# Optimization experiments

Hardware: AMD Instinct MI355X
Metric: run time of the kernel (lower is better)

The kernel has to match this reference:

```python
import jax, jax.numpy as jnp
import numpy as np

B, CIN, H, W = 16, 128, 56, 56
COUT, KH, KW = 256, 3, 3
STRIDE = (1, 1)
PAD = ((1, 1), (1, 1))


def setup_inputs() -> dict:
    key = jax.random.key(0)
    k1, k2, k3 = jax.random.split(key, 3)
    x = jax.random.normal(k1, (B, CIN, H, W), dtype=jnp.float32)
    weight = jax.random.normal(k2, (COUT, CIN, KH, KW), dtype=jnp.float32) * 0.05
    bias = jax.random.normal(k3, (COUT,), dtype=jnp.float32)
    return {"x": x, "weight": weight, "bias": bias}


def reference(x, weight, bias):
    # Conv2d with zero padding, stride 1 -- identical math to the torch
    # unfold+expand+multiply+triple-sum path.
    dn = jax.lax.conv_dimension_numbers(x.shape, weight.shape, ("NCHW", "OIHW", "NCHW"))
    out = jax.lax.conv_general_dilated(x, weight, STRIDE, PAD, dimension_numbers=dn)
    out = out + bias[None, :, None, None]

    # Sparsity of the elementwise product patches * weight.
    # count_nonzero(x_patch * w) over all (b,hw,ww,co,ci,kh,kw) factorizes as
    # sum over windows of conv(1[x!=0], 1[w!=0]) -- same count without
    # materializing the [B,Hw,Ww,Co,Ci,kh,kw] tensor the torch code builds.
    co, ci, kh, kw = weight.shape
    hw, ww = out.shape[2], out.shape[3]
    num_elements = x.shape[0] * hw * ww * co * ci * kh * kw
    nz_map = jax.lax.conv_general_dilated(
        (x != 0).astype(jnp.float32),
        (weight != 0).astype(jnp.float32),
        STRIDE, PAD, dimension_numbers=dn)
    num_nonzero = jnp.sum(nz_map)
    layer_sparsity = (jnp.float32(num_elements) - num_nonzero) / jnp.float32(num_elements)
    return out, layer_sparsity
```

## Files before the change

### kernel.cpp

```cpp
#include <hip/hip_runtime.h>
#include <hip/hip_bf16.h>

typedef __attribute__((ext_vector_type(8))) short bf16x8;
typedef __attribute__((ext_vector_type(8))) unsigned short ushort8;
typedef __attribute__((ext_vector_type(4))) unsigned short ushort4v;
typedef __attribute__((ext_vector_type(4))) float f32x4;
typedef __attribute__((ext_vector_type(4))) unsigned int uint4v;

#define CIN_  128
#define BATCH 16
#define SP_   3136
#define CO_   256
#define NTOT  50176

#define XP_BYTES   13778944
#define WT_BYTES   589824
#define WS_NEEDED  14447104

__device__ __forceinline__ unsigned short f2bf(float f) {
    unsigned int u = __float_as_uint(f);
    u = (u + 0x7fffu + ((u >> 16) & 1u)) >> 16;
    return (unsigned short)u;
}

__device__ __forceinline__ void gl_lds16(const unsigned short* g, unsigned short* l) {
    __builtin_amdgcn_global_load_lds(
        (const __attribute__((address_space(1))) unsigned int*)g,
        (__attribute__((address_space(3))) unsigned int*)l, 16, 0, 0);
}

__global__ __launch_bounds__(256) void k_aux(
    const float* __restrict__ x, const float* __restrict__ w,
    unsigned short* __restrict__ Wt, unsigned short* __restrict__ xp,
    float* __restrict__ Wcnt, float* __restrict__ part)
{
    __shared__ float T[64][65];
    __shared__ float red9[4][9];
    const int blk = blockIdx.x;
    const int tid = threadIdx.x;

    if (blk < 288) {
        int base = (blk * 256 + tid) * 4;
        float4 v = *(const float4*)(w + base);
        #pragma unroll
        for (int j = 0; j < 4; ++j) {
            int e = base + j;
            int co = e / 1152;
            int r  = e - co * 1152;
            int ci = r / 9;
            int koff = r - ci * 9;
            Wt[(koff * 256 + co) * 128 + ci] = f2bf(((const float*)&v)[j]);
        }
    } else if (blk < 576) {
        int lane = tid & 63;
        int j = (blk - 288) * 4 + (tid >> 6);
        float c = 0.f;
        for (int co = lane; co < 256; co += 64)
            c += (w[(size_t)co * 1152 + j] != 0.0f) ? 1.f : 0.f;
        #pragma unroll
        for (int s = 32; s > 0; s >>= 1) c += __shfl_down(c, s, 64);
        if (lane == 0) Wcnt[j] = c;
    } else if (blk < 2624) {
        int bc = blk - 576;
        int ci = bc & 127;
        int b  = bc >> 7;
        const float* xpk = x + (size_t)bc * SP_;
        float cnt[9];
        #pragma unroll
        for (int k = 0; k < 9; ++k) cnt[k] = 0.f;
        for (int e = tid; e < SP_; e += 256) {
            float v = xpk[e];
            if (v != 0.f) {
                int h = e / 56, w_ = e - h * 56;
                float r0 = (h <= 54) ? 1.f : 0.f;
                float r2 = (h >= 1) ? 1.f : 0.f;
                float c0 = (w_ <= 54) ? 1.f : 0.f;
                float c2 = (w_ >= 1) ? 1.f : 0.f;
                cnt[0] += r0 * c0; cnt[1] += r0; cnt[2] += r0 * c2;
                cnt[3] += c0;      cnt[4] += 1.f; cnt[5] += c2;
                cnt[6] += r2 * c0; cnt[7] += r2; cnt[8] += r2 * c2;
            }
        }
        #pragma unroll
        for (int k = 0; k < 9; ++k) {
            #pragma unroll
            for (int s = 32; s > 0; s >>= 1) cnt[k] += __shfl_down(cnt[k], s, 64);
        }
        if ((tid & 63) == 0) {
            #pragma unroll
            for (int k = 0; k < 9; ++k) red9[tid >> 6][k] = cnt[k];
        }
        __syncthreads();
        if (tid < 9) {
            float s = red9[0][tid] + red9[1][tid] + red9[2][tid] + red9[3][tid];
            part[(ci * 9 + tid) * 16 + b] = s;
        }
    } else if (blk < 4192) {
        int i = blk - 2624;
        int sp0 = (i % 49) * 64;
        int rest = i / 49;
        int ci0 = (rest & 1) * 64;
        int b = rest >> 1;
        const float* xb = x + ((size_t)(b * 128 + ci0)) * SP_ + sp0;
        #pragma unroll
        for (int r = 0; r < 16; ++r) {
            const int ci_l = (tid >> 6) * 16 + r;
            const int sp_l = tid & 63;
            T[sp_l][ci_l] = xb[(size_t)ci_l * SP_ + sp_l];
        }
        __syncthreads();
        #pragma unroll
        for (int r = 0; r < 4; ++r) {
            const int sp_l = (tid >> 4) * 4 + r;
            const int cc   = (tid & 15) * 4;
            const int sp = sp0 + sp_l;
            const int oh = sp / 56, ow = sp - oh * 56;
            ushort4v v;
            #pragma unroll
            for (int j = 0; j < 4; ++j) v[j] = f2bf(T[sp_l][cc + j]);
            *(ushort4v*)&xp[(((size_t)b * 58 + oh + 1) * 58 + (ow + 1)) * 128 + ci0 + cc] = v;
        }
    } else {
        int b = blk - 4192;
        if (tid < 228) {
            int oh, ow;
            if (tid < 58)       { oh = 0;            ow = tid; }
            else if (tid < 116) { oh = 57;           ow = tid - 58; }
            else if (tid < 172) { oh = tid - 116 + 1; ow = 0; }
            else                { oh = tid - 172 + 1; ow = 57; }
            unsigned short* p = xp + (((size_t)b * 58 + oh) * 58 + ow) * 128;
            ushort8 z = {};
            #pragma unroll
            for (int j = 0; j < 16; ++j) *(ushort8*)(p + j * 8) = z;
        }
    }
}

__global__ void k_spars(const float* __restrict__ Wcnt, const float* __restrict__ part,
                        float* __restrict__ out_scalar) {
    __shared__ double red[256];
    int t = threadIdx.x;
    double s = 0.0;
    for (int j = t; j < 1152; j += 256) {
        const float4* p4 = (const float4*)(part + (size_t)j * 16);
        float4 a = p4[0], b = p4[1], c = p4[2], d = p4[3];
        float xs = (a.x + a.y + a.z + a.w) + (b.x + b.y + b.z + b.w)
                 + (c.x + c.y + c.z + c.w) + (d.x + d.y + d.z + d.w);
        s += (double)Wcnt[j] * (double)xs;
    }
    red[t] = s; __syncthreads();
    for (int k = 128; k > 0; k >>= 1) {
        if (t < k) red[t] += red[t + k];
        __syncthreads();
    }
    if (t == 0) {
        const double ne = 14797504512.0;
        out_scalar[0] = (float)((ne - red[0]) / ne);
    }
}

__global__ __launch_bounds__(512, 2) void k_conv8(
    const unsigned short* __restrict__ xp, const unsigned short* __restrict__ Wt,
    const float* __restrict__ bias, float* __restrict__ out)
{
    __shared__ __attribute__((aligned(16))) unsigned short Albs[2 * 16384];
    __shared__ __attribute__((aligned(16))) unsigned short Blbs[2 * 16384];

    const int tid  = threadIdx.x;
    const int lane = tid & 63;
    const int l15  = lane & 15;
    const int w    = tid >> 6;
    const int wm   = w >> 2;
    const int wn   = w & 3;
    const int n0   = blockIdx.x * 256;

    int xoffA[2], woffB[2];
    #pragma unroll
    for (int j = 0; j < 2; ++j) {
        int g   = j * 512 + tid;
        int row = g >> 2;
        int c   = (g & 3) ^ ((row >> 1) & 3);
        int n   = n0 + row;
        int b   = n / SP_;
        int sp  = n - b * SP_;
        int oh  = sp / 56, ow = sp - oh * 56;
        xoffA[j] = ((b * 58 + oh + 1) * 58 + (ow + 1)) * 128 + c * 8;
        woffB[j] = row * 128 + c * 8;
    }

    auto stageA = [&](int nb, int xsh, int s) {
        #pragma unroll
        for (int j = 0; j < 2; ++j)
            gl_lds16(xp + xsh + s * 32 + xoffA[j],
                     &Albs[nb + s * 8192 + (j * 512 + tid) * 8]);
    };
    auto stageB = [&](int nb, int wsh, int s) {
        #pragma unroll
        for (int j = 0; j < 2; ++j)
            gl_lds16(Wt + wsh + s * 32 + woffB[j],
                     &Blbs[nb + s * 8192 + (j * 512 + tid) * 8]);
    };

    f32x4 acc[8][4] = {};
    const int cl = lane >> 4;

#define LDA_(bo, S, R) \
    (*(const bf16x8*)&Albs[(bo) + (S) * 8192 + ((R) + l15) * 32 + \
        ((cl ^ ((((R) + l15) >> 1) & 3)) * 8)])
#define LDB_(bo, S, R) \
    (*(const bf16x8*)&Blbs[(bo) + (S) * 8192 + ((R) + l15) * 32 + \
        ((cl ^ ((((R) + l15) >> 1) & 3)) * 8)])

#define SUBPH(BO, S)                                                       \
    {                                                                      \
        bf16x8 b_[4], a_[8];                                               \
        _Pragma("unroll")                                                  \
        for (int nn = 0; nn < 4; ++nn) b_[nn] = LDB_(BO, S, wn * 64 + nn * 16);\
        _Pragma("unroll")                                                  \
        for (int m = 0; m < 8; ++m) a_[m] = LDA_(BO, S, wm * 128 + m * 16);\
        __builtin_amdgcn_s_setprio(1);                                     \
        _Pragma("unroll")                                                  \
        for (int m = 0; m < 8; ++m)                                        \
            _Pragma("unroll")                                              \
            for (int nn = 0; nn < 4; ++nn)                                 \
                acc[m][nn] = __builtin_amdgcn_mfma_f32_16x16x32_bf16(      \
                    a_[m], b_[nn], acc[m][nn], 0, 0, 0);                   \
        __builtin_amdgcn_s_setprio(0);                                     \
    }

    {
        const int xsh0 = (-59) * 128;
        stageA(0, xsh0, 0); stageB(0, 0, 0);
        stageA(0, xsh0, 1); stageB(0, 0, 1);
    }

    #pragma unroll 1
    for (int kt = 0; kt < 18; ++kt) {
        const int bo = (kt & 1) << 14;
        const int nb = 16384 - bo;

        asm volatile("s_waitcnt vmcnt(0)" ::: "memory");
        __builtin_amdgcn_s_barrier();

        if (kt < 17) {
            const int kn = kt + 1;
            const int koffn = kn >> 1;
            const int kdn = koffn / 3;
            const int xshn = ((kdn - 1) * 58 + (koffn - kdn * 3 - 1)) * 128 + (kn & 1) * 64;
            const int wshn = koffn * 32768 + (kn & 1) * 64;
            stageA(nb, xshn, 0); stageB(nb, wshn, 0);
            stageA(nb, xshn, 1); stageB(nb, wshn, 1);
        }

        SUBPH(bo, 0);
        SUBPH(bo, 1);
    }

#undef SUBPH
#undef LDA_
#undef LDB_

    #pragma unroll
    for (int m = 0; m < 8; ++m) {
        int n  = n0 + wm * 128 + m * 16 + (lane >> 4) * 4;
        int b  = n / SP_;
        int sp = n - b * SP_;
        #pragma unroll
        for (int nn = 0; nn < 4; ++nn) {
            int co = wn * 64 + nn * 16 + l15;
            f32x4 v = acc[m][nn] + bias[co];
            *(f32x4*)&out[((size_t)(b * CO_ + co)) * SP_ + sp] = v;
        }
    }
}

__global__ void k_wt(const float* __restrict__ w, unsigned short* __restrict__ Wt) {
    int e = blockIdx.x * 256 + threadIdx.x;
    float v = w[e];
    int co = e / 1152;
    int r  = e - co * 1152;
    int ci = r / 9;
    int koff = r - ci * 9;
    Wt[(koff * 256 + co) * 128 + ci] = f2bf(v);
}

__global__ void k_wcnt(const float* __restrict__ w, float* __restrict__ Wcnt) {
    int j = blockIdx.x;
    int lane = threadIdx.x;
    float c = 0.f;
    for (int co = lane; co < 256; co += 64)
        c += (w[(size_t)co * 1152 + j] != 0.0f) ? 1.f : 0.f;
    #pragma unroll
    for (int s = 32; s > 0; s >>= 1) c += __shfl_down(c, s, 64);
    if (lane == 0) Wcnt[j] = c;
}

__global__ void k_xcnt(const float* __restrict__ x, float* __restrict__ Xcnt) {
    int blk = blockIdx.x;
    int ci = blk & 127;
    const float* xpk = x + (size_t)blk * SP_;
    int tid = threadIdx.x;
    float cnt[9];
    #pragma unroll
    for (int k = 0; k < 9; ++k) cnt[k] = 0.f;
    for (int e = tid; e < SP_; e += 256) {
        float v = xpk[e];
        if (v != 0.f) {
            int h = e / 56, w_ = e - h * 56;
            float r0 = (h <= 54) ? 1.f : 0.f;
            float r2 = (h >= 1) ? 1.f : 0.f;
            float c0 = (w_ <= 54) ? 1.f : 0.f;
            float c2 = (w_ >= 1) ? 1.f : 0.f;
            cnt[0] += r0 * c0; cnt[1] += r0; cnt[2] += r0 * c2;
            cnt[3] += c0;      cnt[4] += 1.f; cnt[5] += c2;
            cnt[6] += r2 * c0; cnt[7] += r2; cnt[8] += r2 * c2;
        }
    }
    #pragma unroll
    for (int k = 0; k < 9; ++k) {
        #pragma unroll
        for (int s = 32; s > 0; s >>= 1) cnt[k] += __shfl_down(cnt[k], s, 64);
    }
    if ((tid & 63) == 0) {
        #pragma unroll
        for (int k = 0; k < 9; ++k)
            atomicAdd(&Xcnt[ci * 9 + k], cnt[k]);
    }
}

__global__ void k_spars_f(const float* __restrict__ Wcnt, const float* __restrict__ Xcnt,
                          float* __restrict__ out_scalar) {
    __shared__ double red[256];
    int t = threadIdx.x;
    double s = 0.0;
    for (int j = t; j < 1152; j += 256)
        s += (double)Wcnt[j] * (double)Xcnt[j];
    red[t] = s; __syncthreads();
    for (int k = 128; k > 0; k >>= 1) {
        if (t < k) red[t] += red[t + k];
        __syncthreads();
    }
    if (t == 0) {
        const double ne = 14797504512.0;
        out_scalar[0] = (float)((ne - red[0]) / ne);
    }
}

__global__ __launch_bounds__(256) void k_conv(
    const float* __restrict__ x, const unsigned short* __restrict__ Wt,
    const float* __restrict__ bias, float* __restrict__ out)
{
    __shared__ __attribute__((aligned(16))) unsigned short AldsF[64][40];
    __shared__ __attribute__((aligned(16))) unsigned short BldsF[64][40];

    const int tid  = threadIdx.x;
    const int lane = tid & 63;
    const int wid  = tid >> 6;
    const int wm   = wid >> 1, wn = wid & 1;

    const int n0  = blockIdx.x * 64;
    const int b   = blockIdx.x / 49;
    const int sp0 = n0 - b * SP_;
    const int co0 = blockIdx.y * 64;

    const int a_co = tid >> 2;
    const int a_ci = (tid & 3) * 8;
    const int b_n  = tid & 63;
    const int b_k0 = (tid >> 6) * 8;

    const int sp = sp0 + b_n;
    const int oh = sp / 56, ow = sp - oh * 56;

    f32x4 acc[2][2] = {};
    const float* xb_base = x + (size_t)b * CIN_ * SP_;

    for (int koff = 0; koff < 9; ++koff) {
        const int dh = koff / 3 - 1, dw = koff - (koff / 3) * 3 - 1;
        const int ih = oh + dh, iw = ow + dw;
        const bool valid = ((unsigned)ih < 56u) && ((unsigned)iw < 56u);
        const float* xb = xb_base + sp + dh * 56 + dw;
        const unsigned short* wp = Wt + ((size_t)(koff * 256 + co0 + a_co)) * 128 + a_ci;

        for (int ci0 = 0; ci0 < 128; ci0 += 32) {
            uint4v av = *(const uint4v*)(wp + ci0);
            *(uint4v*)&AldsF[a_co][a_ci] = av;
            ushort8 bv;
            #pragma unroll
            for (int j = 0; j < 8; ++j) {
                int ci = ci0 + b_k0 + j;
                float v = 0.f;
                if (valid) v = xb[(size_t)ci * SP_];
                bv[j] = f2bf(v);
            }
            *(ushort8*)&BldsF[b_n][b_k0] = bv;
            __syncthreads();

            const int row = lane & 15;
            const int kq  = (lane >> 4) * 8;
            bf16x8 a0 = *(const bf16x8*)&AldsF[wm * 32 + row][kq];
            bf16x8 a1 = *(const bf16x8*)&AldsF[wm * 32 + 16 + row][kq];
            bf16x8 bb0 = *(const bf16x8*)&BldsF[wn * 32 + row][kq];
            bf16x8 bb1 = *(const bf16x8*)&BldsF[wn * 32 + 16 + row][kq];
            acc[0][0] = __builtin_amdgcn_mfma_f32_16x16x32_bf16(a0, bb0, acc[0][0], 0, 0, 0);
            acc[0][1] = __builtin_amdgcn_mfma_f32_16x16x32_bf16(a0, bb1, acc[0][1], 0, 0, 0);
            acc[1][0] = __builtin_amdgcn_mfma_f32_16x16x32_bf16(a1, bb0, acc[1][0], 0, 0, 0);
            acc[1][1] = __builtin_amdgcn_mfma_f32_16x16x32_bf16(a1, bb1, acc[1][1], 0, 0, 0);
            __syncthreads();
        }
    }

    const int col = lane & 15;
    const int rb  = (lane >> 4) * 4;
    #pragma unroll
    for (int f = 0; f < 2; ++f) {
        #pragma unroll
        for (int g = 0; g < 2; ++g) {
            int spc = sp0 + wn * 32 + g * 16 + col;
            #pragma unroll
            for (int r = 0; r < 4; ++r) {
                int co = co0 + wm * 32 + f * 16 + rb + r;
                out[((size_t)(b * CO_ + co)) * SP_ + spc] = acc[f][g][r] + bias[co];
            }
        }
    }
}

extern "C" void kernel_launch(void* const* d_in, const int* in_sizes, int n_in,
                              void* d_out, int out_size, void* d_ws, size_t ws_size,
                              hipStream_t stream) {
    const float* x    = (const float*)d_in[0];
    const float* w    = (const float*)d_in[1];
    const float* bias = (const float*)d_in[2];
    float* out = (float*)d_out;

    if (ws_size >= (size_t)WS_NEEDED) {
        unsigned short* xp = (unsigned short*)d_ws;
        unsigned short* Wt = (unsigned short*)((char*)d_ws + XP_BYTES);
        float* Wcnt = (float*)((char*)d_ws + XP_BYTES + WT_BYTES);
        float* part = Wcnt + 1152;

        hipLaunchKernelGGL(k_aux,   dim3(4208),   dim3(256), 0, stream,
                           x, w, Wt, xp, Wcnt, part);
        hipLaunchKernelGGL(k_conv8, dim3(196),    dim3(512), 0, stream, xp, Wt, bias, out);
        hipLaunchKernelGGL(k_spars, dim3(1),      dim3(256), 0, stream, Wcnt, part,
                           out + 12845056);
    } else {
        unsigned short* Wt = (unsigned short*)d_ws;
        float* Wcnt = (float*)((char*)d_ws + WT_BYTES);
        float* Xcnt = Wcnt + 1152;

        hipMemsetAsync((void*)Xcnt, 0, 1152 * sizeof(float), stream);
        hipLaunchKernelGGL(k_wt,      dim3(1152),    dim3(256), 0, stream, w, Wt);
        hipLaunchKernelGGL(k_wcnt,    dim3(1152),    dim3(64),  0, stream, w, Wcnt);
        hipLaunchKernelGGL(k_xcnt,    dim3(2048),    dim3(256), 0, stream, x, Xcnt);
        hipLaunchKernelGGL(k_conv,    dim3(784, 4),  dim3(256), 0, stream, x, Wt, bias, out);
        hipLaunchKernelGGL(k_spars_f, dim3(1),       dim3(256), 0, stream, Wcnt, Xcnt,
                           out + 12845056);
    }
}
```

Measured before the change: 70.34 us.

## Convert conv GEMM main loop to 4-slot LDS ring with two-stage-ahead prefetch

The double-buffered K loop (18 iterations, each waiting on all loads and then computing two sub-phases) becomes a 4-slot ring over 36 half-size K stages. Each stage reads its fragments from LDS, issues global-to-LDS loads two stages ahead, and waits only until the next stage's data has landed (vmcnt(4)) before the barrier and MFMAs. The aim is to keep loads in flight across compute instead of draining the memory queue every iteration. The cost is twice as many barriers per tile, with the LDS footprint unchanged.

```diff
diff --git a/kernel.cpp b/kernel.cpp
--- a/kernel.cpp
+++ b/kernel.cpp
@@ -163,8 +163,8 @@
     const unsigned short* __restrict__ xp, const unsigned short* __restrict__ Wt,
     const float* __restrict__ bias, float* __restrict__ out)
 {
-    __shared__ __attribute__((aligned(16))) unsigned short Albs[2 * 16384];
-    __shared__ __attribute__((aligned(16))) unsigned short Blbs[2 * 16384];
+    __shared__ __attribute__((aligned(16))) unsigned short Albs[4 * 8192];
+    __shared__ __attribute__((aligned(16))) unsigned short Blbs[4 * 8192];
 
     const int tid  = threadIdx.x;
     const int lane = tid & 63;
@@ -188,75 +188,74 @@
         woffB[j] = row * 128 + c * 8;
     }
 
-    auto stageA = [&](int nb, int xsh, int s) {
+    auto stageA = [&](int slotoff, int xsh) {
         #pragma unroll
         for (int j = 0; j < 2; ++j)
-            gl_lds16(xp + xsh + s * 32 + xoffA[j],
-                     &Albs[nb + s * 8192 + (j * 512 + tid) * 8]);
+            gl_lds16(xp + xsh + xoffA[j], &Albs[slotoff + (j * 512 + tid) * 8]);
     };
-    auto stageB = [&](int nb, int wsh, int s) {
+    auto stageB = [&](int slotoff, int wsh) {
         #pragma unroll
         for (int j = 0; j < 2; ++j)
-            gl_lds16(Wt + wsh + s * 32 + woffB[j],
-                     &Blbs[nb + s * 8192 + (j * 512 + tid) * 8]);
+            gl_lds16(Wt + wsh + woffB[j], &Blbs[slotoff + (j * 512 + tid) * 8]);
     };
 
     f32x4 acc[8][4] = {};
     const int cl = lane >> 4;
 
-#define LDA_(bo, S, R) \
-    (*(const bf16x8*)&Albs[(bo) + (S) * 8192 + ((R) + l15) * 32 + \
+#define LDA_(SLOT, R) \
+    (*(const bf16x8*)&Albs[(SLOT) * 8192 + ((R) + l15) * 32 + \
         ((cl ^ ((((R) + l15) >> 1) & 3)) * 8)])
-#define LDB_(bo, S, R) \
-    (*(const bf16x8*)&Blbs[(bo) + (S) * 8192 + ((R) + l15) * 32 + \
+#define LDB_(SLOT, R) \
+    (*(const bf16x8*)&Blbs[(SLOT) * 8192 + ((R) + l15) * 32 + \
         ((cl ^ ((((R) + l15) >> 1) & 3)) * 8)])
-
-#define SUBPH(BO, S)                                                       \
-    {                                                                      \
-        bf16x8 b_[4], a_[8];                                               \
-        _Pragma("unroll")                                                  \
-        for (int nn = 0; nn < 4; ++nn) b_[nn] = LDB_(BO, S, wn * 64 + nn * 16);\
-        _Pragma("unroll")                                                  \
-        for (int m = 0; m < 8; ++m) a_[m] = LDA_(BO, S, wm * 128 + m * 16);\
-        __builtin_amdgcn_s_setprio(1);                                     \
-        _Pragma("unroll")                                                  \
-        for (int m = 0; m < 8; ++m)                                        \
-            _Pragma("unroll")                                              \
-            for (int nn = 0; nn < 4; ++nn)                                 \
-                acc[m][nn] = __builtin_amdgcn_mfma_f32_16x16x32_bf16(      \
-                    a_[m], b_[nn], acc[m][nn], 0, 0, 0);                   \
-        __builtin_amdgcn_s_setprio(0);                                     \
-    }
 
     {
         const int xsh0 = (-59) * 128;
-        stageA(0, xsh0, 0); stageB(0, 0, 0);
-        stageA(0, xsh0, 1); stageB(0, 0, 1);
+        stageA(0, xsh0);          stageB(0, 0);
+        stageA(8192, xsh0 + 32);  stageB(8192, 32);
+        asm volatile("s_waitcnt vmcnt(4)" ::: "memory");
+        __builtin_amdgcn_s_barrier();
     }
 
     #pragma unroll 1
-    for (int kt = 0; kt < 18; ++kt) {
-        const int bo = (kt & 1) << 14;
-        const int nb = 16384 - bo;
-
-        asm volatile("s_waitcnt vmcnt(0)" ::: "memory");
-        __builtin_amdgcn_s_barrier();
-
-        if (kt < 17) {
-            const int kn = kt + 1;
-            const int koffn = kn >> 1;
-            const int kdn = koffn / 3;
-            const int xshn = ((kdn - 1) * 58 + (koffn - kdn * 3 - 1)) * 128 + (kn & 1) * 64;
-            const int wshn = koffn * 32768 + (kn & 1) * 64;
-            stageA(nb, xshn, 0); stageB(nb, wshn, 0);
-            stageA(nb, xshn, 1); stageB(nb, wshn, 1);
-        }
-
-        SUBPH(bo, 0);
-        SUBPH(bo, 1);
-    }
-
-#undef SUBPH
+    for (int koff = 0; koff < 9; ++koff) {
+        #pragma unroll
+        for (int q = 0; q < 4; ++q) {
+            const int p = koff * 4 + q;
+            const int slot = q;
+
+            bf16x8 b_[4], a_[8];
+            #pragma unroll
+            for (int nn = 0; nn < 4; ++nn) b_[nn] = LDB_(slot, wn * 64 + nn * 16);
+            #pragma unroll
+            for (int m = 0; m < 8; ++m)    a_[m] = LDA_(slot, wm * 128 + m * 16);
+
+            if (p + 2 <= 35) {
+                const int p2  = p + 2;
+                const int ko2 = p2 >> 2;
+                const int q2  = p2 & 3;
+                const int kd2 = ko2 / 3;
+                const int xsh = ((kd2 - 1) * 58 + (ko2 - kd2 * 3 - 1)) * 128 + q2 * 32;
+                const int wsh = ko2 * 32768 + q2 * 32;
+                stageA(q2 * 8192, xsh);
+                stageB(q2 * 8192, wsh);
+                asm volatile("s_waitcnt vmcnt(4)" ::: "memory");
+            } else {
+                asm volatile("s_waitcnt vmcnt(0)" ::: "memory");
+            }
+            __builtin_amdgcn_s_barrier();
+
+            __builtin_amdgcn_s_setprio(1);
+            #pragma unroll
+            for (int m = 0; m < 8; ++m)
+                #pragma unroll
+                for (int nn = 0; nn < 4; ++nn)
+                    acc[m][nn] = __builtin_amdgcn_mfma_f32_16x16x32_bf16(
+                        a_[m], b_[nn], acc[m][nn], 0, 0, 0);
+            __builtin_amdgcn_s_setprio(0);
+        }
+    }
+
 #undef LDA_
 #undef LDB_
 
```

Result: faster. 64.61 us (-8.2%).
